# Performance work log

Measured on AMD Instinct MI355X. Metric: run time of the kernel, lower is better.

The kernel has to match this reference:

```python
import math
import jax, jax.numpy as jnp
import numpy as np

N_WL = 262144
T_REF = 273.15          # CONSTANTS.STANDARD_TEMPERATURE [K]
P_REF = 101325.0        # CONSTANTS.STANDARD_PRESSURE [Pa]
C_LIGHT = 2.99792458e8  # CONSTANTS.SPEED_OF_LIGHT
K_B = 1.380649e-23      # CONSTANTS.BOLTZMANN
N_AVO = 6.02214076e23   # CONSTANTS.AVOGADRO

# hard-coded line database: [center_wl, strength, width, temp_exp]; rows 0-2 O3, 3-5 H2O, 6-9 CO2
LINES = np.array([
    [254.0, 1.15e-17, 2.0, 0.05], [280.0, 5e-18, 3.0, 0.04], [310.0, 1.9e-19, 2.5, 0.03],
    [940.0, 2.5e-23, 3.0, 0.4],  [1130.0, 8.2e-24, 2.5, 0.35], [1380.0, 1.8e-22, 4.0, 0.45],
    [1400.0, 3.5e-25, 3.0, 0.5], [1600.0, 7.8e-26, 2.5, 0.48], [2000.0, 4.2e-24, 4.0, 0.52],
    [2700.0, 1.2e-24, 3.5, 0.49]], dtype=np.float32)
MASS = np.array([48.0]*3 + [18.0]*3 + [44.0]*4, dtype=np.float32)


def setup_inputs() -> dict:
    key = jax.random.key(0)
    ks = jax.random.split(key, 8)
    inp = {
        'wavelengths': jnp.linspace(200.0, 3000.0, N_WL, dtype=jnp.float32),
        'temperature': jnp.float32(250.0),
        'pressure': jnp.float32(80000.0),
        'conc_o3': jnp.float32(1e-6),
        'conc_h2o': jnp.float32(1e-2),
        'conc_co2': jnp.float32(4e-4),
        'mix_w1': jax.random.normal(ks[0], (10, 64), jnp.float32) * 0.3,
        'mix_b1': jnp.zeros((64,), jnp.float32),
        'mix_w2': jax.random.normal(ks[1], (64, 64), jnp.float32) * 0.12,
        'mix_b2': jnp.zeros((64,), jnp.float32),
        'mix_w3': jax.random.normal(ks[2], (64, N_WL), jnp.float32) * 0.12,
        'mix_b3': jnp.zeros((N_WL,), jnp.float32),
        'cont_w1': jax.random.normal(ks[3], (5, 32), jnp.float32) * 0.4,
        'cont_b1': jnp.zeros((32,), jnp.float32),
        'cont_w2': jax.random.normal(ks[4], (32, N_WL), jnp.float32) * 0.17,
        'cont_b2': jnp.zeros((N_WL,), jnp.float32),
    }
    return inp


def _voigt(wl, nu0, gamma_L, gamma_D):
    # wl: [N]; nu0, gamma_L, gamma_D: [L] -> returns [L, N]
    sigma = gamma_D / (math.sqrt(2.0 * math.log(2.0)) + 1e-12)          # [L]
    x = (wl[None, :] - nu0[:, None]) / (sigma[:, None] + 1e-12)          # [L,N]
    y = (gamma_L / (sigma + 1e-12))[:, None]                             # [L,1]
    t = y - 1j * x
    s = jnp.abs(x) + y
    mask1 = s >= 15.0
    mask2 = (s < 15.0) & (jnp.abs(x) >= 5.5)
    w1 = (t * 0.5641896 / (0.5 + t ** 2)).real
    u = t ** 2
    w2 = (t * (1.410474 + u * 0.5641896) / (0.75 + u * (3.0 + u))).real
    w3 = (jnp.exp(-x ** 2) * jnp.cos(2.0 * x * y) / math.sqrt(math.pi)
          + 2.0 * y / math.pi * jnp.sin(x ** 2) / (x ** 2 + y ** 2 + 1e-10))
    result = jnp.where(mask1, w1, jnp.where(mask2, w2, w3))
    return result / (sigma[:, None] * math.sqrt(math.pi) + 1e-12)


def reference(wavelengths, temperature, pressure, conc_o3, conc_h2o, conc_co2,
              mix_w1, mix_b1, mix_w2, mix_b2, mix_w3, mix_b3,
              cont_w1, cont_b1, cont_w2, cont_b2):
    lines = jnp.asarray(LINES)
    mass = jnp.asarray(MASS)
    conc = jnp.stack([conc_o3, conc_o3, conc_o3,
                      conc_h2o, conc_h2o, conc_h2o,
                      conc_co2, conc_co2, conc_co2, conc_co2])          # [10]
    nu0, strength, width, temp_exp = lines[:, 0], lines[:, 1], lines[:, 2], lines[:, 3]
    strength_T = strength * (T_REF / (temperature + 1e-12)) ** temp_exp  # [10]
    gamma_L = width * (pressure / (P_REF + 1e-12)) * jnp.sqrt(T_REF / (temperature + 1e-12))
    gamma_D = nu0 / C_LIGHT * jnp.sqrt(2.0 * K_B * temperature * N_AVO / (mass + 1e-12))

    profiles = _voigt(wavelengths, nu0, gamma_L, gamma_D)                # [10,N]
    cross = jnp.sum((conc * strength_T)[:, None] * profiles, axis=0)     # [N]

    # continuum net: 5 -> 32 (SiLU) -> N (softplus)
    cont_feat = jnp.stack([temperature / (T_REF + 1e-12),
                           pressure / (P_REF + 1e-12),
                           conc_h2o,
                           jnp.float32(1.0), jnp.float32(0.0)])
    h = jax.nn.silu(cont_feat @ cont_w1 + cont_b1)
    continuum = jax.nn.softplus(h @ cont_w2 + cont_b2)
    cross = cross + continuum

    # line-mixing net: 10 -> 64 (SiLU) -> 64 (SiLU) -> N (sigmoid); dropout is eval-mode identity
    mix_feat = jnp.concatenate([jnp.stack([temperature / (T_REF + 1e-12),
                                           pressure / (P_REF + 1e-12)]),
                                cross[:8]])
    m = jax.nn.silu(mix_feat @ mix_w1 + mix_b1)
    m = jax.nn.silu(m @ mix_w2 + mix_b2)
    mixing = jax.nn.sigmoid(m @ mix_w3 + mix_b3)
    return cross * (1.0 + 0.1 * (mixing - 0.5))
```

## Files before the change

kernel.cpp:

```cpp
#include <hip/hip_runtime.h>
#include <math.h>

#define N_WL 262144

#define T_REF 273.15
#define P_REF 101325.0
#define C_LIGHT 299792458.0
#define K_B 1.380649e-23
#define N_AVO 6.02214076e+23

__constant__ float c_nu0[10]  = {254.0f, 280.0f, 310.0f, 940.0f, 1130.0f, 1380.0f, 1400.0f, 1600.0f, 2000.0f, 2700.0f};
__constant__ float c_str[10]  = {1.15e-17f, 5e-18f, 1.9e-19f, 2.5e-23f, 8.2e-24f, 1.8e-22f, 3.5e-25f, 7.8e-26f, 4.2e-24f, 1.2e-24f};
__constant__ float c_wid[10]  = {2.0f, 3.0f, 2.5f, 3.0f, 2.5f, 4.0f, 3.0f, 2.5f, 4.0f, 3.5f};
__constant__ float c_texp[10] = {0.05f, 0.04f, 0.03f, 0.4f, 0.35f, 0.45f, 0.5f, 0.48f, 0.52f, 0.49f};
__constant__ float c_mass[10] = {48.f, 48.f, 48.f, 18.f, 18.f, 18.f, 44.f, 44.f, 44.f, 44.f};
__constant__ int   c_cidx[10] = {0, 0, 0, 1, 1, 1, 2, 2, 2, 2};

__device__ __forceinline__ float siluf(float x)     { return x / (1.0f + __expf(-x)); }
__device__ __forceinline__ float sigmoidf(float x)  { return 1.0f / (1.0f + __expf(-x)); }
__device__ __forceinline__ float softplusf(float x) { return fmaxf(x, 0.0f) + log1pf(expf(-fabsf(x))); }

__device__ __forceinline__ float voigt_w(float x, float y) {
    float ax = fabsf(x);
    float s  = ax + y;
    if (s >= 15.0f) {
        float ur = y * y - x * x;
        float ui = -2.0f * x * y;
        float dr = 0.5f + ur, di = ui;
        float nr = 0.5641896f * y, ni = 0.5641896f * (-x);
        float den = dr * dr + di * di;
        return (nr * dr + ni * di) / den;
    } else if (ax >= 5.5f) {
        float ur = y * y - x * x;
        float ui = -2.0f * x * y;
        float pr = 1.410474f + 0.5641896f * ur;
        float pi_ = 0.5641896f * ui;
        float tr = y, ti = -x;
        float nr = tr * pr - ti * pi_;
        float ni = tr * pi_ + ti * pr;
        float u2r = ur * ur - ui * ui;
        float u2i = 2.0f * ur * ui;
        float dr = 0.75f + 3.0f * ur + u2r;
        float di = 3.0f * ui + u2i;
        float den = dr * dr + di * di;
        return (nr * dr + ni * di) / den;
    } else {
        float x2 = x * x;
        return expf(-x2) * cosf(2.0f * x * y) * 0.5641895835477563f
             + (2.0f * y / 3.14159265358979f) * sinf(x2) / (x2 + y * y + 1e-10f);
    }
}

__global__ __launch_bounds__(256) void GasAbs_fused_kernel(
    const float* __restrict__ wl,
    const float* __restrict__ Tp, const float* __restrict__ Pp,
    const float* __restrict__ o3, const float* __restrict__ h2o, const float* __restrict__ co2,
    const float* __restrict__ mix_w1, const float* __restrict__ mix_b1,
    const float* __restrict__ mix_w2, const float* __restrict__ mix_b2,
    const float* __restrict__ mix_w3, const float* __restrict__ mix_b3,
    const float* __restrict__ cont_w1, const float* __restrict__ cont_b1,
    const float* __restrict__ cont_w2, const float* __restrict__ cont_b2,
    float* __restrict__ out)
{
    __shared__ float s_nu0[10], s_isig[10], s_y[10], s_scale[10];
    __shared__ float s_h[32];
    __shared__ float s_feat[10];
    __shared__ float s_m1[64];
    __shared__ float s_m2[64];

    const int t = threadIdx.x;

    if (t < 10) {
        const double T = (double)Tp[0];
        const double P = (double)Pp[0];
        const float cc3[3] = {o3[0], h2o[0], co2[0]};
        double nu0 = (double)c_nu0[t];
        double sT  = (double)c_str[t] * pow(T_REF / (T + 1e-12), (double)c_texp[t]);
        double gL  = (double)c_wid[t] * (P / (P_REF + 1e-12)) * sqrt(T_REF / (T + 1e-12));
        double gD  = nu0 / C_LIGHT * sqrt(2.0 * K_B * T * N_AVO / ((double)c_mass[t] + 1e-12));
        double sig = gD / (sqrt(2.0 * log(2.0)) + 1e-12);
        s_nu0[t]   = (float)nu0;
        s_isig[t]  = (float)(1.0 / (sig + 1e-12));
        s_y[t]     = (float)(gL / (sig + 1e-12));
        s_scale[t] = (float)((double)cc3[c_cidx[t]] * sT / (sig * sqrt(M_PI) + 1e-12));
    }
    if (t < 32) {
        const double T = (double)Tp[0];
        const double P = (double)Pp[0];
        float cf[5];
        cf[0] = (float)(T / (T_REF + 1e-12));
        cf[1] = (float)(P / (P_REF + 1e-12));
        cf[2] = h2o[0];
        cf[3] = 1.0f;
        cf[4] = 0.0f;
        float a = cont_b1[t];
        #pragma unroll
        for (int k = 0; k < 5; k++) a = fmaf(cf[k], cont_w1[k * 32 + t], a);
        s_h[t] = siluf(a);
    }
    __syncthreads();

    if (t < 8) {
        float w = wl[t];
        float c = cont_b2[t];
        #pragma unroll
        for (int j = 0; j < 32; j++) c = fmaf(s_h[j], cont_w2[(size_t)j * N_WL + t], c);
        float cross = softplusf(c);
        #pragma unroll
        for (int l = 0; l < 10; l++) {
            float x = (w - s_nu0[l]) * s_isig[l];
            cross = fmaf(s_scale[l], voigt_w(x, s_y[l]), cross);
        }
        s_feat[2 + t] = cross;
    }
    if (t == 0) {
        const double T = (double)Tp[0];
        const double P = (double)Pp[0];
        s_feat[0] = (float)(T / (T_REF + 1e-12));
        s_feat[1] = (float)(P / (P_REF + 1e-12));
    }
    __syncthreads();

    if (t < 64) {
        float a = mix_b1[t];
        #pragma unroll
        for (int k = 0; k < 10; k++) a = fmaf(s_feat[k], mix_w1[k * 64 + t], a);
        s_m1[t] = siluf(a);
    }
    __syncthreads();

    if (t < 64) {
        float a = mix_b2[t];
        #pragma unroll
        for (int k = 0; k < 64; k++) a = fmaf(s_m1[k], mix_w2[k * 64 + t], a);
        s_m2[t] = siluf(a);
    }
    __syncthreads();

    const int i = blockIdx.x * 256 + t;
    const float* __restrict__ wp = cont_w2 + i;
    const float* __restrict__ mp = mix_w3  + i;

    const float wv = wl[i];
    const float bc = cont_b2[i];
    const float bm = mix_b3[i];

    float buf[16];
    #pragma unroll
    for (int k = 0; k < 16; k++)
        buf[k] = wp[(size_t)k * N_WL];
    asm volatile("" ::: "memory");

    float vsum = 0.0f;
    #pragma unroll
    for (int l = 0; l < 10; l++) {
        const float x = (wv - s_nu0[l]) * s_isig[l];
        vsum = fmaf(s_scale[l], voigt_w(x, s_y[l]), vsum);
    }

    float acc_c = bc;
    float acc_m = bm;

    #pragma unroll
    for (int g = 0; g < 12; g++) {
        #pragma unroll
        for (int u = 0; u < 8; u++) {
            const int k = g * 8 + u;
            const float v = buf[k & 15];
            if (k < 32) acc_c = fmaf(s_h[k],      v, acc_c);
            else        acc_m = fmaf(s_m2[k - 32], v, acc_m);
            const int kn = k + 16;
            if (kn < 96)
                buf[k & 15] = (kn < 32) ? wp[(size_t)kn * N_WL]
                                        : mp[(size_t)(kn - 32) * N_WL];
        }
        asm volatile("" ::: "memory");
    }

    const float cross = softplusf(acc_c) + vsum;
    out[i] = cross * (0.95f + 0.1f * sigmoidf(acc_m));
}

extern "C" void kernel_launch(void* const* d_in, const int* in_sizes, int n_in,
                              void* d_out, int out_size, void* d_ws, size_t ws_size,
                              hipStream_t stream) {
    const float* wl      = (const float*)d_in[0];
    const float* Tp      = (const float*)d_in[1];
    const float* Pp      = (const float*)d_in[2];
    const float* o3      = (const float*)d_in[3];
    const float* h2o     = (const float*)d_in[4];
    const float* co2     = (const float*)d_in[5];
    const float* mix_w1  = (const float*)d_in[6];
    const float* mix_b1  = (const float*)d_in[7];
    const float* mix_w2  = (const float*)d_in[8];
    const float* mix_b2  = (const float*)d_in[9];
    const float* mix_w3  = (const float*)d_in[10];
    const float* mix_b3  = (const float*)d_in[11];
    const float* cont_w1 = (const float*)d_in[12];
    const float* cont_b1 = (const float*)d_in[13];
    const float* cont_w2 = (const float*)d_in[14];
    const float* cont_b2 = (const float*)d_in[15];
    float* out = (float*)d_out;

    const int threads = 256;
    const int blocks  = N_WL / threads;
    GasAbs_fused_kernel<<<blocks, threads, 0, stream>>>(
        wl, Tp, Pp, o3, h2o, co2,
        mix_w1, mix_b1, mix_w2, mix_b2, mix_w3, mix_b3,
        cont_w1, cont_b1, cont_w2, cont_b2, out);
}
```

Before: 150.8 us.

## Split weight reduction across lane quarters with float4 loads and shuffle reduce

Remaps each wavefront so that 16 lanes each own four consecutive wavelengths, loaded as float4. The 96-deep weight reduction is split across four lane quarters, and the partial sums are combined with xor shuffles. This targets fewer, wider memory transactions on the bandwidth-heavy weight streaming and adds an occupancy hint to launch bounds. In exchange, every quarter recomputes the full Voigt profile for its four wavelengths, which makes the transcendental-heavy line-shape work four times redundant. It also adds shuffle overhead.

```diff
diff --git a/kernel.cpp b/kernel.cpp
--- a/kernel.cpp
+++ b/kernel.cpp
@@ -51,7 +51,7 @@
     }
 }
 
-__global__ __launch_bounds__(256) void GasAbs_fused_kernel(
+__global__ __launch_bounds__(256, 4) void GasAbs_fused_kernel(
     const float* __restrict__ wl,
     const float* __restrict__ Tp, const float* __restrict__ Pp,
     const float* __restrict__ o3, const float* __restrict__ h2o, const float* __restrict__ co2,
@@ -137,48 +137,89 @@
     }
     __syncthreads();
 
-    const int i = blockIdx.x * 256 + t;
-    const float* __restrict__ wp = cont_w2 + i;
-    const float* __restrict__ mp = mix_w3  + i;
-
-    const float wv = wl[i];
-    const float bc = cont_b2[i];
-    const float bm = mix_b3[i];
-
-    float buf[16];
+    const int lane = t & 63;
+    const int q    = lane >> 4;
+    const int sub  = lane & 15;
+    const int wv_  = t >> 6;
+    const int i0   = (blockIdx.x * 4 + wv_) * 64 + sub * 4;
+
+    const float* baseA = cont_w2 + (size_t)(q * 8)  * N_WL + i0;
+    const float* baseB = mix_w3  + (size_t)(q * 16) * N_WL + i0;
+
+    const float4 w4  = *reinterpret_cast<const float4*>(wl + i0);
+    const float4 bc4 = *reinterpret_cast<const float4*>(cont_b2 + i0);
+    const float4 bm4 = *reinterpret_cast<const float4*>(mix_b3 + i0);
+
+    float4 buf[8];
     #pragma unroll
-    for (int k = 0; k < 16; k++)
-        buf[k] = wp[(size_t)k * N_WL];
+    for (int k = 0; k < 8; k++)
+        buf[k] = *reinterpret_cast<const float4*>(baseA + (size_t)k * N_WL);
     asm volatile("" ::: "memory");
 
-    float vsum = 0.0f;
+    float vs0 = 0.0f, vs1 = 0.0f, vs2 = 0.0f, vs3 = 0.0f;
     #pragma unroll
     for (int l = 0; l < 10; l++) {
-        const float x = (wv - s_nu0[l]) * s_isig[l];
-        vsum = fmaf(s_scale[l], voigt_w(x, s_y[l]), vsum);
-    }
-
-    float acc_c = bc;
-    float acc_m = bm;
+        const float nu0 = s_nu0[l], isig = s_isig[l], yy = s_y[l], sc = s_scale[l];
+        vs0 = fmaf(sc, voigt_w((w4.x - nu0) * isig, yy), vs0);
+        vs1 = fmaf(sc, voigt_w((w4.y - nu0) * isig, yy), vs1);
+        vs2 = fmaf(sc, voigt_w((w4.z - nu0) * isig, yy), vs2);
+        vs3 = fmaf(sc, voigt_w((w4.w - nu0) * isig, yy), vs3);
+    }
+
+    float4 accA = {0.f, 0.f, 0.f, 0.f};
+    float4 accB = {0.f, 0.f, 0.f, 0.f};
 
     #pragma unroll
-    for (int g = 0; g < 12; g++) {
-        #pragma unroll
-        for (int u = 0; u < 8; u++) {
-            const int k = g * 8 + u;
-            const float v = buf[k & 15];
-            if (k < 32) acc_c = fmaf(s_h[k],      v, acc_c);
-            else        acc_m = fmaf(s_m2[k - 32], v, acc_m);
-            const int kn = k + 16;
-            if (kn < 96)
-                buf[k & 15] = (kn < 32) ? wp[(size_t)kn * N_WL]
-                                        : mp[(size_t)(kn - 32) * N_WL];
+    for (int g = 0; g < 6; g++) {
+        #pragma unroll
+        for (int u = 0; u < 4; u++) {
+            const int k = g * 4 + u;
+            const float4 v = buf[k & 7];
+            if (k < 8) {
+                const float cf = s_h[q * 8 + k];
+                accA.x = fmaf(cf, v.x, accA.x);
+                accA.y = fmaf(cf, v.y, accA.y);
+                accA.z = fmaf(cf, v.z, accA.z);
+                accA.w = fmaf(cf, v.w, accA.w);
+            } else {
+                const float cf = s_m2[q * 16 + (k - 8)];
+                accB.x = fmaf(cf, v.x, accB.x);
+                accB.y = fmaf(cf, v.y, accB.y);
+                accB.z = fmaf(cf, v.z, accB.z);
+                accB.w = fmaf(cf, v.w, accB.w);
+            }
+            const int kn = k + 8;
+            if (kn < 24) {
+                buf[k & 7] = (kn < 8)
+                    ? *reinterpret_cast<const float4*>(baseA + (size_t)kn * N_WL)
+                    : *reinterpret_cast<const float4*>(baseB + (size_t)(kn - 8) * N_WL);
+            }
         }
         asm volatile("" ::: "memory");
     }
 
-    const float cross = softplusf(acc_c) + vsum;
-    out[i] = cross * (0.95f + 0.1f * sigmoidf(acc_m));
+    accA.x += __shfl_xor(accA.x, 16); accA.x += __shfl_xor(accA.x, 32);
+    accA.y += __shfl_xor(accA.y, 16); accA.y += __shfl_xor(accA.y, 32);
+    accA.z += __shfl_xor(accA.z, 16); accA.z += __shfl_xor(accA.z, 32);
+    accA.w += __shfl_xor(accA.w, 16); accA.w += __shfl_xor(accA.w, 32);
+    accB.x += __shfl_xor(accB.x, 16); accB.x += __shfl_xor(accB.x, 32);
+    accB.y += __shfl_xor(accB.y, 16); accB.y += __shfl_xor(accB.y, 32);
+    accB.z += __shfl_xor(accB.z, 16); accB.z += __shfl_xor(accB.z, 32);
+    accB.w += __shfl_xor(accB.w, 16); accB.w += __shfl_xor(accB.w, 32);
+
+    float4 o;
+    {
+        const float cr0 = softplusf(bc4.x + accA.x) + vs0;
+        const float cr1 = softplusf(bc4.y + accA.y) + vs1;
+        const float cr2 = softplusf(bc4.z + accA.z) + vs2;
+        const float cr3 = softplusf(bc4.w + accA.w) + vs3;
+        o.x = cr0 * (0.95f + 0.1f * sigmoidf(bm4.x + accB.x));
+        o.y = cr1 * (0.95f + 0.1f * sigmoidf(bm4.y + accB.y));
+        o.z = cr2 * (0.95f + 0.1f * sigmoidf(bm4.z + accB.z));
+        o.w = cr3 * (0.95f + 0.1f * sigmoidf(bm4.w + accB.w));
+    }
+    if (q == 0)
+        *reinterpret_cast<float4*>(out + i0) = o;
 }
 
 extern "C" void kernel_launch(void* const* d_in, const int* in_sizes, int n_in,
@@ -203,7 +244,7 @@
     float* out = (float*)d_out;
 
     const int threads = 256;
-    const int blocks  = N_WL / threads;
+    const int blocks  = N_WL / 256;
     GasAbs_fused_kernel<<<blocks, threads, 0, stream>>>(
         wl, Tp, Pp, o3, h2o, co2,
         mix_w1, mix_b1, mix_w2, mix_b2, mix_w3, mix_b3,
```

Result: slower. 155.6 us (+3.2%).

## Stage weight tiles into LDS via global_load_lds in a persistent grid

Applied to the files above, without the earlier changes.

Replaces the per-thread strided register prefetch of the 96 weight rows with a 96x128 LDS tile. Each wave fills the tile using 16-byte direct global-to-LDS loads, and threads then read their column from shared memory. The launch becomes a fixed 512-block, 128-thread grid-stride loop, so the per-block MLP prologue is paid once for several tiles instead of once per 256 outputs. Loads and compute are not double-buffered, and the 48KB LDS tile limits how many blocks fit on a CU.

```diff
diff --git a/kernel.cpp b/kernel.cpp
--- a/kernel.cpp
+++ b/kernel.cpp
@@ -19,6 +19,13 @@
 __device__ __forceinline__ float siluf(float x)     { return x / (1.0f + __expf(-x)); }
 __device__ __forceinline__ float sigmoidf(float x)  { return 1.0f / (1.0f + __expf(-x)); }
 __device__ __forceinline__ float softplusf(float x) { return fmaxf(x, 0.0f) + log1pf(expf(-fabsf(x))); }
+
+__device__ __forceinline__ void stage16(const float* g, float* l) {
+    __builtin_amdgcn_global_load_lds(
+        (const __attribute__((address_space(1))) void*)g,
+        (__attribute__((address_space(3))) void*)l,
+        16, 0, 0);
+}
 
 __device__ __forceinline__ float voigt_w(float x, float y) {
     float ax = fabsf(x);
@@ -51,7 +58,7 @@
     }
 }
 
-__global__ __launch_bounds__(256) void GasAbs_fused_kernel(
+__global__ __launch_bounds__(128) void GasAbs_fused_kernel(
     const float* __restrict__ wl,
     const float* __restrict__ Tp, const float* __restrict__ Pp,
     const float* __restrict__ o3, const float* __restrict__ h2o, const float* __restrict__ co2,
@@ -62,6 +69,7 @@
     const float* __restrict__ cont_w2, const float* __restrict__ cont_b2,
     float* __restrict__ out)
 {
+    __shared__ float s_w[96][128];
     __shared__ float s_nu0[10], s_isig[10], s_y[10], s_scale[10];
     __shared__ float s_h[32];
     __shared__ float s_feat[10];
@@ -137,48 +145,55 @@
     }
     __syncthreads();
 
-    const int i = blockIdx.x * 256 + t;
-    const float* __restrict__ wp = cont_w2 + i;
-    const float* __restrict__ mp = mix_w3  + i;
-
-    const float wv = wl[i];
-    const float bc = cont_b2[i];
-    const float bm = mix_b3[i];
-
-    float buf[16];
-    #pragma unroll
-    for (int k = 0; k < 16; k++)
-        buf[k] = wp[(size_t)k * N_WL];
-    asm volatile("" ::: "memory");
-
-    float vsum = 0.0f;
-    #pragma unroll
-    for (int l = 0; l < 10; l++) {
-        const float x = (wv - s_nu0[l]) * s_isig[l];
-        vsum = fmaf(s_scale[l], voigt_w(x, s_y[l]), vsum);
-    }
-
-    float acc_c = bc;
-    float acc_m = bm;
-
-    #pragma unroll
-    for (int g = 0; g < 12; g++) {
-        #pragma unroll
-        for (int u = 0; u < 8; u++) {
-            const int k = g * 8 + u;
-            const float v = buf[k & 15];
-            if (k < 32) acc_c = fmaf(s_h[k],      v, acc_c);
-            else        acc_m = fmaf(s_m2[k - 32], v, acc_m);
-            const int kn = k + 16;
-            if (kn < 96)
-                buf[k & 15] = (kn < 32) ? wp[(size_t)kn * N_WL]
-                                        : mp[(size_t)(kn - 32) * N_WL];
+    const int wid  = t >> 6;
+    const int lane = t & 63;
+    const int half = lane >> 5;
+    const int col  = (lane & 31) * 4;
+
+    for (int tile = blockIdx.x; tile < N_WL / 128; tile += gridDim.x) {
+        const int i0 = tile * 128;
+
+        {
+            const int j0 = wid * 48;
+            #pragma unroll
+            for (int r = 0; r < 24; ++r) {
+                const int j  = j0 + r * 2;
+                const int jr = j + half;
+                const float* gb = (jr < 32)
+                    ? cont_w2 + (size_t)jr * N_WL
+                    : mix_w3 + (size_t)(jr - 32) * N_WL;
+                stage16(gb + i0 + col, &s_w[j][0]);
+            }
         }
-        asm volatile("" ::: "memory");
-    }
-
-    const float cross = softplusf(acc_c) + vsum;
-    out[i] = cross * (0.95f + 0.1f * sigmoidf(acc_m));
+
+        const int i = i0 + t;
+        const float wv = wl[i];
+        const float bc = cont_b2[i];
+        const float bm = mix_b3[i];
+
+        __syncthreads();
+
+        float acc_c = bc;
+        #pragma unroll
+        for (int j = 0; j < 32; ++j)
+            acc_c = fmaf(s_h[j], s_w[j][t], acc_c);
+
+        float acc_m = bm;
+        #pragma unroll
+        for (int j = 0; j < 64; ++j)
+            acc_m = fmaf(s_m2[j], s_w[32 + j][t], acc_m);
+
+        float vsum = 0.0f;
+        #pragma unroll
+        for (int l = 0; l < 10; l++) {
+            const float x = (wv - s_nu0[l]) * s_isig[l];
+            vsum = fmaf(s_scale[l], voigt_w(x, s_y[l]), vsum);
+        }
+
+        out[i] = (softplusf(acc_c) + vsum) * (0.95f + 0.1f * sigmoidf(acc_m));
+
+        __syncthreads();
+    }
 }
 
 extern "C" void kernel_launch(void* const* d_in, const int* in_sizes, int n_in,
@@ -202,9 +217,7 @@
     const float* cont_b2 = (const float*)d_in[15];
     float* out = (float*)d_out;
 
-    const int threads = 256;
-    const int blocks  = N_WL / threads;
-    GasAbs_fused_kernel<<<blocks, threads, 0, stream>>>(
+    GasAbs_fused_kernel<<<512, 128, 0, stream>>>(
         wl, Tp, Pp, o3, h2o, co2,
         mix_w1, mix_b1, mix_w2, mix_b2, mix_w3, mix_b3,
         cont_w1, cont_b1, cont_w2, cont_b2, out);
```

After: 158.5 us. 1.05x slower.
